# Kernel tuning notes

Measured on AMD Instinct MI355X. Metric: run time of the kernel, lower is better.

## Reference

```python
import jax, jax.numpy as jnp
import numpy as np

L, B, C, H = 1024, 8, 1024, 16
D = C // H  # 64


def setup_inputs() -> dict:
    key = jax.random.key(0)
    ks = jax.random.split(key, 8)
    hidden_states = jax.random.normal(ks[0], (L, B, C), dtype=jnp.float32)
    rotary_pos_emb = jax.random.uniform(ks[1], (L, D // 2), dtype=jnp.float32) * 10.0
    attention_mask = jax.random.randint(ks[2], (B, L, L), 0, 2) > 0
    s = 1.0 / np.sqrt(C)
    Wqkv = jax.random.uniform(ks[3], (3 * C, C), dtype=jnp.float32, minval=-s, maxval=s)
    bqkv = jax.random.uniform(ks[4], (3 * C,), dtype=jnp.float32, minval=-s, maxval=s)
    Wo = jax.random.uniform(ks[5], (C, C), dtype=jnp.float32, minval=-s, maxval=s)
    bo = jax.random.uniform(ks[6], (C,), dtype=jnp.float32, minval=-s, maxval=s)
    return {"hidden_states": hidden_states, "rotary_pos_emb": rotary_pos_emb,
            "attention_mask": attention_mask, "Wqkv": Wqkv, "bqkv": bqkv, "Wo": Wo, "bo": bo}


def _rotate_half(x):
    # interleaved pairs: [-x1, x0, -x3, x2, ...]
    x2 = x.reshape(*x.shape[:-1], -1, 2)
    return jnp.stack((-x2[..., 1], x2[..., 0]), axis=-1).reshape(x.shape)


def reference(hidden_states, rotary_pos_emb, attention_mask, Wqkv, bqkv, Wo, bo):
    Lx, Bx, Cx = hidden_states.shape
    # QKV projection: (L,B,3C) -> (3,B,L,H,D)
    qkv = hidden_states @ Wqkv.T + bqkv
    qkv = qkv.reshape(Lx, Bx, 3, H, D).transpose(2, 1, 0, 3, 4)
    q, k, v = qkv[0], qkv[1], qkv[2]  # (B, L, H, D)
    # RoPE: freqs (L, D/2) -> cos/sin (1, L, 1, D) via duplication
    rpe = rotary_pos_emb[None] if rotary_pos_emb.ndim == 2 else rotary_pos_emb
    cos = jnp.concatenate([jnp.cos(rpe), jnp.cos(rpe)], axis=-1)[:, :, None, :]
    sin = jnp.concatenate([jnp.sin(rpe), jnp.sin(rpe)], axis=-1)[:, :, None, :]
    q = q * cos + _rotate_half(q) * sin
    k = k * cos + _rotate_half(k) * sin
    # (B, H, L, D)
    q = q.transpose(0, 2, 1, 3)
    k = k.transpose(0, 2, 1, 3)
    v = v.transpose(0, 2, 1, 3)
    scale = 1.0 / jnp.sqrt(jnp.asarray(D, dtype=q.dtype))
    scores = jnp.einsum('bhqd,bhkd->bhqk', q, k) * scale
    # torch SDPA bool mask: True = attend, False = masked
    scores = jnp.where(attention_mask[:, None, :, :], scores, jnp.finfo(scores.dtype).min)
    attn = jax.nn.softmax(scores, axis=-1)
    out = jnp.einsum('bhqk,bhkd->bhqd', attn, v)  # (B, H, L, D)
    out = out.transpose(2, 0, 1, 3).reshape(Lx, Bx, Cx)  # (L, B, C)
    return out @ Wo.T + bo
```

## Files before the change

### kernel.cpp

```cpp
#include <hip/hip_runtime.h>
#include <hip/hip_bf16.h>

typedef short bf16x8 __attribute__((ext_vector_type(8)));
typedef short bf16x4 __attribute__((ext_vector_type(4)));
typedef float f32x4 __attribute__((ext_vector_type(4)));
typedef unsigned int u32;
typedef unsigned long long u64;

#define GLD_LDS16(gp, lp) \
  __builtin_amdgcn_global_load_lds((const __attribute__((address_space(1))) u32*)(gp), \
                                   (__attribute__((address_space(3))) u32*)(lp), 16, 0, 0)

__device__ __forceinline__ short f2bf(float f) {
  u32 u = __builtin_bit_cast(u32, f);
  u = (u + 0x7fffu + ((u >> 16) & 1u)) >> 16;
  return (short)u;
}

__device__ __forceinline__ u32 pack2_bf16(float a, float b) {
#if __has_builtin(__builtin_amdgcn_cvt_pk_bf16_f32)
  typedef __bf16 bf16v2 __attribute__((ext_vector_type(2)));
  bf16v2 r = __builtin_amdgcn_cvt_pk_bf16_f32(a, b);
  return __builtin_bit_cast(u32, r);
#else
  u32 r;
  asm("v_cvt_pk_bf16_f32 %0, %1, %2" : "=v"(r) : "v"(a), "v"(b));
  return r;
#endif
}

__device__ __forceinline__ float exp2_fast(float x) {
#if __has_builtin(__builtin_amdgcn_exp2f)
  return __builtin_amdgcn_exp2f(x);
#else
  return exp2f(x);
#endif
}


__global__ __launch_bounds__(256) void cvt_all(
    const float* __restrict__ hs, const float* __restrict__ wqkv,
    const float* __restrict__ wo, short* __restrict__ xb,
    short* __restrict__ wqkvb, short* __restrict__ wob) {
  int b = blockIdx.x;
  const float* in;
  short* out;
  int base;
  if (b < 8192) {
    in = hs; out = xb; base = b * 1024;
  } else if (b < 8192 + 3072) {
    in = wqkv; out = wqkvb; base = (b - 8192) * 1024;
  } else {
    in = wo; out = wob; base = (b - 11264) * 1024;
  }
  int i = base + threadIdx.x * 4;
  float4 v = *(const float4*)(in + i);
  short4 o;
  o.x = f2bf(v.x); o.y = f2bf(v.y); o.z = f2bf(v.z); o.w = f2bf(v.w);
  *(short4*)(out + i) = o;
}

__global__ void rope_tables(const float* __restrict__ rpe, float* __restrict__ cosT,
                            float* __restrict__ sinT) {
  int i = blockIdx.x * 256 + threadIdx.x;
  float v = rpe[i];
  cosT[i] = cosf(v);
  sinT[i] = sinf(v);
}

__global__ void mask_pack(const int* __restrict__ m, u64* __restrict__ out) {
  int i = blockIdx.x * 256 + threadIdx.x;
  u64 bm = __ballot(m[i] != 0);
  if ((threadIdx.x & 63) == 0) out[i >> 6] = bm;
}

__global__ __launch_bounds__(256, 4) void gemm_qkv(
    const short* __restrict__ Xb, const short* __restrict__ Wb,
    const float* __restrict__ bqkv, const float* __restrict__ cosT,
    const float* __restrict__ sinT, short* __restrict__ qb,
    short* __restrict__ kbuf, short* __restrict__ vbuf) {
  __shared__ short Ash[2][128 * 32];
  __shared__ short Bsh[2][128 * 32];
  const int tid = threadIdx.x;
  const int wid = tid >> 6, lane = tid & 63;
  const int g = lane >> 4, c = lane & 15;
  const int wm = wid >> 1, wn = wid & 1;
  const int m0 = blockIdx.y * 128, n0 = blockIdx.x * 128;

  f32x4 acc[4][4];
  for (int i = 0; i < 4; i++)
    for (int j = 0; j < 4; j++) acc[i][j] = (f32x4){0.f, 0.f, 0.f, 0.f};

  const int srow = lane >> 2;
  const int scol = ((lane & 3) ^ ((lane >> 3) & 3)) * 8;
  const short* AgL = Xb + (long)(m0 + wid * 32 + srow) * 1024 + scol;
  const short* BgL = Wb + (long)(n0 + wid * 32 + srow) * 1024 + scol;
  const int dst0 = (wid * 32) * 32;
  const int dst1 = (wid * 32 + 16) * 32;
  const int ck = g ^ ((c >> 1) & 3);

#define QKV_KSTEP(CA, CB, PA, PB, nko) do { \
    GLD_LDS16(AgL + (nko), &(PA)[dst0]); \
    GLD_LDS16(AgL + (nko) + 16 * 1024, &(PA)[dst1]); \
    GLD_LDS16(BgL + (nko), &(PB)[dst0]); \
    GLD_LDS16(BgL + (nko) + 16 * 1024, &(PB)[dst1]); \
    asm volatile("s_waitcnt vmcnt(4)" ::: "memory"); \
    __builtin_amdgcn_s_barrier(); \
    __builtin_amdgcn_sched_barrier(0); \
    bf16x8 af[4], bfr[4]; \
    for (int i = 0; i < 4; i++) \
      af[i] = *(const bf16x8*)&(CA)[(wm * 64 + i * 16 + c) * 32 + ck * 8]; \
    for (int j = 0; j < 4; j++) \
      bfr[j] = *(const bf16x8*)&(CB)[(wn * 64 + j * 16 + c) * 32 + ck * 8]; \
    for (int i = 0; i < 4; i++) \
      for (int j = 0; j < 4; j++) \
        acc[i][j] = __builtin_amdgcn_mfma_f32_16x16x32_bf16(bfr[j], af[i], acc[i][j], 0, 0, 0); \
    __builtin_amdgcn_sched_barrier(0); \
    __builtin_amdgcn_s_barrier(); \
  } while (0)

  GLD_LDS16(AgL, &Ash[0][dst0]);
  GLD_LDS16(AgL + 16 * 1024, &Ash[0][dst1]);
  GLD_LDS16(BgL, &Bsh[0][dst0]);
  GLD_LDS16(BgL + 16 * 1024, &Bsh[0][dst1]);
  for (int kt = 0; kt < 32; kt += 2) {
    QKV_KSTEP(Ash[0], Bsh[0], Ash[1], Bsh[1], (kt + 1) * 32);
    QKV_KSTEP(Ash[1], Bsh[1], Ash[0], Bsh[0], ((kt + 2) & 31) * 32);
  }
#undef QKV_KSTEP

  for (int jt = 0; jt < 4; jt++) {
    const int chan = n0 + wn * 64 + jt * 16 + g * 4;
    const int three = chan >> 10;
    const int hh = (chan >> 6) & 15;
    const int d = chan & 63;
    const float4 bq = *(const float4*)&bqkv[chan];
    for (int i = 0; i < 4; i++) {
      const int r = m0 + wm * 64 + i * 16 + c;
      const int l = r >> 3, b = r & 7;
      float v0 = acc[i][jt][0] + bq.x;
      float v1 = acc[i][jt][1] + bq.y;
      float v2 = acc[i][jt][2] + bq.z;
      float v3 = acc[i][jt][3] + bq.w;
      const long doff = ((long)(b * 16 + hh) * 1024 + l) * 64 + d;
      if (three == 2) {
        uint2 o = {pack2_bf16(v0, v1), pack2_bf16(v2, v3)};
        *(uint2*)&vbuf[doff] = o;
      } else {
        const float4 cs = *(const float4*)&cosT[l * 32 + (d & 31)];
        const float4 sn = *(const float4*)&sinT[l * 32 + (d & 31)];
        float e0 = v0 * cs.x - v1 * sn.x;
        float o0 = v1 * cs.y + v0 * sn.y;
        float e1 = v2 * cs.z - v3 * sn.z;
        float o1 = v3 * cs.w + v2 * sn.w;
        short* dst;
        if (three == 0) {
          const float S = 0.18033688011f;
          e0 *= S; o0 *= S; e1 *= S; o1 *= S;
          dst = qb;
        } else {
          dst = kbuf;
        }
        uint2 o = {pack2_bf16(e0, o0), pack2_bf16(e1, o1)};
        *(uint2*)&dst[doff] = o;
      }
    }
  }
}

__global__ __launch_bounds__(256) void transpose_v(const short* __restrict__ vbuf,
                                                   short* __restrict__ vTb) {
  __shared__ short T[64 * 72];
  const int bh = blockIdx.y;
  const int l0 = blockIdx.x * 64;
  const int t = threadIdx.x;
  const int row = t >> 3;
  const int cc = (t & 7) * 8;
  const short* src = vbuf + ((long)bh * 1024 + l0) * 64;
  for (int p = 0; p < 2; p++) {
    int lr = row + p * 32;
    *(bf16x8*)&T[lr * 72 + cc] = *(const bf16x8*)&src[(long)lr * 64 + cc];
  }
  __syncthreads();
  short* dst = vTb + (long)bh * 64 * 1024 + l0;
  for (int p = 0; p < 2; p++) {
    int d = row + p * 32;
    bf16x8 v;
    for (int j = 0; j < 8; j++) v[j] = T[(cc + j) * 72 + d];
    *(bf16x8*)&dst[(long)d * 1024 + cc] = v;
  }
}

__global__ __launch_bounds__(256, 5) void flash_attn(
    const short* __restrict__ qb, const short* __restrict__ kbuf,
    const short* __restrict__ vTb, const u64* __restrict__ maskb,
    short* __restrict__ attno) {
  __shared__ short K0[64 * 64], K1[64 * 64];
  __shared__ short V0[64 * 64], V1[64 * 64];
  const int t = threadIdx.x;
  const int wid = t >> 6, lane = t & 63;
  const int g = lane >> 4, c = lane & 15;
  const int q0 = blockIdx.x * 64;
  const int bh = blockIdx.y;
  const int b = bh >> 4;
  const int h = bh & 15;
  const long qoff = (long)bh * 1024 * 64;
  const int qrow = q0 + wid * 16 + c;

  bf16x8 aq0, aq1;
  {
    const short* qp = qb + qoff + (long)qrow * 64;
    aq0 = *(const bf16x8*)(qp + g * 8);
    aq1 = *(const bf16x8*)(qp + 32 + g * 8);
  }

  f32x4 Od[4];
  for (int i = 0; i < 4; i++) Od[i] = (f32x4){0.f, 0.f, 0.f, 0.f};
  f32x4 Ld = (f32x4){0.f, 0.f, 0.f, 0.f};
  float m_run = -1e30f;

  bf16x8 avOnes8;
  {
    union { bf16x8 v; u32 u[4]; } av;
    u32 o1 = (c == 0) ? 0x3F803F80u : 0u;
    av.u[0] = av.u[1] = av.u[2] = av.u[3] = o1;
    avOnes8 = av.v;
  }

  const u64* mrow = maskb + ((long)b * 1024 + qrow) * 16;
  const short* Kg = kbuf + qoff;
  const short* Vg = vTb + qoff;

  const int l8 = lane >> 3, l7 = lane & 7;
  const int sr = wid * 16 + l8;
  const int sch = ((l7 ^ l8) & 7) * 8;
  const int r1 = wid * 16 + l8;
  const int r2 = r1 + 8;
  const int kp1 = (r1 & 32) | (((r1 & 15) >> 2) << 3) | (((r1 >> 4) & 1) << 2) | (r1 & 3);
  const int kp2 = (r2 & 32) | (((r2 & 15) >> 2) << 3) | (((r2 >> 4) & 1) << 2) | (r2 & 3);

  const int ck0 = g ^ (c & 7);
  const int kOff0 = c * 64 + ck0 * 8;
  const int kOff1 = c * 64 + (ck0 ^ 4) * 8;
  int vOff32[2];
  for (int kg = 0; kg < 2; kg++)
    vOff32[kg] = c * 64 + (((kg * 4 + g) ^ (c & 7)) * 8);

#define STAGE(KD, VD, ktn) do { \
    GLD_LDS16(Kg + (long)((ktn) + kp1) * 64 + sch,      &KD[(wid * 16) * 64]); \
    GLD_LDS16(Kg + (long)((ktn) + kp2) * 64 + sch,      &KD[(wid * 16 + 8) * 64]); \
    GLD_LDS16(Vg + (long)sr * 1024 + (ktn) + sch,       &VD[(wid * 16) * 64]); \
    GLD_LDS16(Vg + (long)(sr + 8) * 1024 + (ktn) + sch, &VD[(wid * 16 + 8) * 64]); \
  } while (0)

#define TILE(KB, VB, KP, VP, ki) do { \
    u64 mw = mrow[ki];  \
    __syncthreads();  \
    STAGE(KP, VP, (((ki) + 1) & 15) * 64); \
    f32x4 z[4]; \
    for (int nt = 0; nt < 4; nt++) { \
      bf16x8 bk0 = *(const bf16x8*)&KB[kOff0 + nt * 1024]; \
      bf16x8 bk1 = *(const bf16x8*)&KB[kOff1 + nt * 1024]; \
      f32x4 zz = (f32x4){0.f, 0.f, 0.f, 0.f}; \
      zz = __builtin_amdgcn_mfma_f32_16x16x32_bf16(bk0, aq0, zz, 0, 0, 0); \
      zz = __builtin_amdgcn_mfma_f32_16x16x32_bf16(bk1, aq1, zz, 0, 0, 0); \
      z[nt] = zz; \
    } \
    float mx = fmaxf(fmaxf(fmaxf(z[0][0], z[0][1]), fmaxf(z[0][2], z[0][3])), \
                     fmaxf(fmaxf(z[1][0], z[1][1]), fmaxf(z[1][2], z[1][3]))); \
    mx = fmaxf(mx, fmaxf(fmaxf(fmaxf(z[2][0], z[2][1]), fmaxf(z[2][2], z[2][3])), \
                         fmaxf(fmaxf(z[3][0], z[3][1]), fmaxf(z[3][2], z[3][3])))); \
    if (__ballot(mx > m_run + 8.f)) {  \
      mx = fmaxf(mx, __shfl_xor(mx, 16, 64)); \
      mx = fmaxf(mx, __shfl_xor(mx, 32, 64)); \
      float mnew = fmaxf(m_run, mx); \
      float al = exp2_fast(m_run - mnew); \
      for (int dt = 0; dt < 4; dt++) { \
        Od[dt][0] *= al; Od[dt][1] *= al; Od[dt][2] *= al; Od[dt][3] *= al; \
      } \
      Ld[0] *= al; \
      m_run = mnew; \
    } \
    for (int kg = 0; kg < 2; kg++) { \
      union { bf16x8 v; u32 u[4]; } pu; \
      for (int ntp = 0; ntp < 2; ntp++) { \
        const int nt = kg * 2 + ntp; \
        u32 m4 = (u32)(mw >> (kg * 32 + g * 8 + ntp * 4)) & 0xFu; \
        u32 mlo = ((m4 & 1u) ? 0xFFFFu : 0u) | ((m4 & 2u) ? 0xFFFF0000u : 0u); \
        u32 mhi = ((m4 & 4u) ? 0xFFFFu : 0u) | ((m4 & 8u) ? 0xFFFF0000u : 0u); \
        float p0 = exp2_fast(z[nt][0] - m_run); \
        float p1 = exp2_fast(z[nt][1] - m_run); \
        float p2 = exp2_fast(z[nt][2] - m_run); \
        float p3 = exp2_fast(z[nt][3] - m_run); \
        pu.u[ntp * 2 + 0] = pack2_bf16(p0, p1) & mlo; \
        pu.u[ntp * 2 + 1] = pack2_bf16(p2, p3) & mhi; \
      } \
      Ld = __builtin_amdgcn_mfma_f32_16x16x32_bf16(avOnes8, pu.v, Ld, 0, 0, 0); \
      for (int dt = 0; dt < 4; dt++) { \
        bf16x8 av = *(const bf16x8*)&VB[vOff32[kg] + dt * 1024]; \
        Od[dt] = __builtin_amdgcn_mfma_f32_16x16x32_bf16(av, pu.v, Od[dt], 0, 0, 0); \
      } \
    } \
  } while (0)

  STAGE(K0, V0, 0);
  for (int ki = 0; ki < 16; ki += 2) {
    TILE(K0, V0, K1, V1, ki);
    TILE(K1, V1, K0, V0, ki + 1);
  }
#undef TILE
#undef STAGE

  float lsum = __shfl(Ld[0], c, 64);
  float inv = 1.f / lsum;
  long rbase = ((long)qrow * 8 + b) * 1024 + h * 64 + g * 4;
  for (int dt = 0; dt < 4; dt++) {
    union { bf16x4 v; u32 u[2]; } o;
    o.u[0] = pack2_bf16(Od[dt][0] * inv, Od[dt][1] * inv);
    o.u[1] = pack2_bf16(Od[dt][2] * inv, Od[dt][3] * inv);
    *(bf16x4*)&attno[rbase + dt * 16] = o.v;
  }
}

__global__ __launch_bounds__(256, 4) void gemm_out(
    const short* __restrict__ Ab, const short* __restrict__ Wob,
    const float* __restrict__ bo, float* __restrict__ out) {
  __shared__ short Ash[2][128 * 32];
  __shared__ short Bsh[2][128 * 32];
  const int tid = threadIdx.x;
  const int wid = tid >> 6, lane = tid & 63;
  const int g = lane >> 4, c = lane & 15;
  const int wm = wid >> 1, wn = wid & 1;
  const int m0 = blockIdx.y * 128, n0 = blockIdx.x * 128;

  f32x4 acc[4][4];
  for (int i = 0; i < 4; i++)
    for (int j = 0; j < 4; j++) acc[i][j] = (f32x4){0.f, 0.f, 0.f, 0.f};

  const int srow = lane >> 2;
  const int scol = ((lane & 3) ^ ((lane >> 3) & 3)) * 8;
  const short* AgL = Ab + (long)(m0 + wid * 32 + srow) * 1024 + scol;
  const short* BgL = Wob + (long)(n0 + wid * 32 + srow) * 1024 + scol;
  const int dst0 = (wid * 32) * 32;
  const int dst1 = (wid * 32 + 16) * 32;
  const int ck = g ^ ((c >> 1) & 3);

#define OUT_KSTEP(CA, CB, PA, PB, nko) do { \
    GLD_LDS16(AgL + (nko), &(PA)[dst0]); \
    GLD_LDS16(AgL + (nko) + 16 * 1024, &(PA)[dst1]); \
    GLD_LDS16(BgL + (nko), &(PB)[dst0]); \
    GLD_LDS16(BgL + (nko) + 16 * 1024, &(PB)[dst1]); \
    asm volatile("s_waitcnt vmcnt(4)" ::: "memory"); \
    __builtin_amdgcn_s_barrier(); \
    __builtin_amdgcn_sched_barrier(0); \
    bf16x8 af[4], bfr[4]; \
    for (int i = 0; i < 4; i++) \
      af[i] = *(const bf16x8*)&(CA)[(wm * 64 + i * 16 + c) * 32 + ck * 8]; \
    for (int j = 0; j < 4; j++) \
      bfr[j] = *(const bf16x8*)&(CB)[(wn * 64 + j * 16 + c) * 32 + ck * 8]; \
    for (int i = 0; i < 4; i++) \
      for (int j = 0; j < 4; j++) \
        acc[i][j] = __builtin_amdgcn_mfma_f32_16x16x32_bf16(af[i], bfr[j], acc[i][j], 0, 0, 0); \
    __builtin_amdgcn_sched_barrier(0); \
    __builtin_amdgcn_s_barrier(); \
  } while (0)

  GLD_LDS16(AgL, &Ash[0][dst0]);
  GLD_LDS16(AgL + 16 * 1024, &Ash[0][dst1]);
  GLD_LDS16(BgL, &Bsh[0][dst0]);
  GLD_LDS16(BgL + 16 * 1024, &Bsh[0][dst1]);
  for (int kt = 0; kt < 32; kt += 2) {
    OUT_KSTEP(Ash[0], Bsh[0], Ash[1], Bsh[1], (kt + 1) * 32);
    OUT_KSTEP(Ash[1], Bsh[1], Ash[0], Bsh[0], ((kt + 2) & 31) * 32);
  }
#undef OUT_KSTEP

  for (int jt = 0; jt < 4; jt++) {
    const int j = n0 + wn * 64 + jt * 16 + c;
    const float bias = bo[j];
    for (int i = 0; i < 4; i++) {
      const int rbase = m0 + wm * 64 + i * 16 + g * 4;
      for (int reg = 0; reg < 4; reg++)
        out[(long)(rbase + reg) * 1024 + j] = acc[i][jt][reg] + bias;
    }
  }
}

extern "C" void kernel_launch(void* const* d_in, const int* in_sizes, int n_in,
                              void* d_out, int out_size, void* d_ws, size_t ws_size,
                              hipStream_t stream) {
  const float* hs = (const float*)d_in[0];
  const float* rpe = (const float*)d_in[1];
  const int* amask = (const int*)d_in[2];
  const float* Wqkv = (const float*)d_in[3];
  const float* bqkv = (const float*)d_in[4];
  const float* Wo = (const float*)d_in[5];
  const float* bo = (const float*)d_in[6];
  float* out = (float*)d_out;

  char* ws = (char*)d_ws;
  auto alloc = [&](size_t bytes) {
    char* p = ws;
    ws += (bytes + 255) & ~(size_t)255;
    return p;
  };
  short* Xb = (short*)alloc(8192LL * 1024 * 2);
  short* Wqkvb = (short*)alloc(3072LL * 1024 * 2);
  short* Wob = (short*)alloc(1024LL * 1024 * 2);
  float* cosT = (float*)alloc(1024 * 32 * 4);
  float* sinT = (float*)alloc(1024 * 32 * 4);
  u64* maskb = (u64*)alloc(8LL * 1024 * 16 * 8);
  short* qb = (short*)alloc(128LL * 1024 * 64 * 2);
  short* kbuf = (short*)alloc(128LL * 1024 * 64 * 2);
  short* vbuf = (short*)alloc(128LL * 1024 * 64 * 2);
  short* vTb = (short*)alloc(128LL * 1024 * 64 * 2);
  short* attno = (short*)alloc(8192LL * 1024 * 2);

  cvt_all<<<12288, 256, 0, stream>>>(hs, Wqkv, Wo, Xb, Wqkvb, Wob);
  rope_tables<<<128, 256, 0, stream>>>(rpe, cosT, sinT);
  mask_pack<<<32768, 256, 0, stream>>>(amask, maskb);
  gemm_qkv<<<dim3(24, 64), 256, 0, stream>>>(Xb, Wqkvb, bqkv, cosT, sinT, qb, kbuf, vbuf);
  transpose_v<<<dim3(16, 128), 256, 0, stream>>>(vbuf, vTb);
  flash_attn<<<dim3(16, 128), 256, 0, stream>>>(qb, kbuf, vTb, maskb, attno);
  gemm_out<<<dim3(8, 64), 256, 0, stream>>>(attno, Wob, bo, out);
}
```

Baseline: 326.4 us.

## Fuse prep kernels, swizzle block order, and restructure GEMM LDS pipelining

Merges the three preprocessing kernels (mask packing, bf16 conversion, RoPE tables) into one launch to cut launch overhead. Remaps block indices in both GEMMs and the attention kernel with an XCD-style swizzle (bid&7 stride) so that blocks sharing operands land on the same die's L2. Replaces the hand-tuned vmcnt wait plus raw barrier double buffer in the GEMMs with a stage/compute split separated by __syncthreads. That split may serialize load completion more conservatively, because __syncthreads drains all outstanding loads.

```diff
diff --git a/kernel.cpp b/kernel.cpp
--- a/kernel.cpp
+++ b/kernel.cpp
@@ -37,41 +37,44 @@
 #endif
 }
 
-
-__global__ __launch_bounds__(256) void cvt_all(
+__global__ __launch_bounds__(256) void prep_all(
+    const int* __restrict__ m, u64* __restrict__ maskb,
     const float* __restrict__ hs, const float* __restrict__ wqkv,
     const float* __restrict__ wo, short* __restrict__ xb,
-    short* __restrict__ wqkvb, short* __restrict__ wob) {
+    short* __restrict__ wqkvb, short* __restrict__ wob,
+    const float* __restrict__ rpe, float* __restrict__ cosT,
+    float* __restrict__ sinT) {
   int b = blockIdx.x;
-  const float* in;
-  short* out;
-  int base;
-  if (b < 8192) {
-    in = hs; out = xb; base = b * 1024;
-  } else if (b < 8192 + 3072) {
-    in = wqkv; out = wqkvb; base = (b - 8192) * 1024;
-  } else {
-    in = wo; out = wob; base = (b - 11264) * 1024;
-  }
-  int i = base + threadIdx.x * 4;
-  float4 v = *(const float4*)(in + i);
-  short4 o;
-  o.x = f2bf(v.x); o.y = f2bf(v.y); o.z = f2bf(v.z); o.w = f2bf(v.w);
-  *(short4*)(out + i) = o;
-}
-
-__global__ void rope_tables(const float* __restrict__ rpe, float* __restrict__ cosT,
-                            float* __restrict__ sinT) {
-  int i = blockIdx.x * 256 + threadIdx.x;
+  if (b < 32768) {
+    int i = b * 256 + threadIdx.x;
+    u64 bm = __ballot(m[i] != 0);
+    if ((threadIdx.x & 63) == 0) maskb[i >> 6] = bm;
+    return;
+  }
+  b -= 32768;
+  if (b < 12288) {
+    const float* in;
+    short* out;
+    int base;
+    if (b < 8192) {
+      in = hs; out = xb; base = b * 1024;
+    } else if (b < 8192 + 3072) {
+      in = wqkv; out = wqkvb; base = (b - 8192) * 1024;
+    } else {
+      in = wo; out = wob; base = (b - 11264) * 1024;
+    }
+    int i = base + threadIdx.x * 4;
+    float4 v = *(const float4*)(in + i);
+    short4 o;
+    o.x = f2bf(v.x); o.y = f2bf(v.y); o.z = f2bf(v.z); o.w = f2bf(v.w);
+    *(short4*)(out + i) = o;
+    return;
+  }
+  b -= 12288;
+  int i = b * 256 + threadIdx.x;
   float v = rpe[i];
   cosT[i] = cosf(v);
   sinT[i] = sinf(v);
-}
-
-__global__ void mask_pack(const int* __restrict__ m, u64* __restrict__ out) {
-  int i = blockIdx.x * 256 + threadIdx.x;
-  u64 bm = __ballot(m[i] != 0);
-  if ((threadIdx.x & 63) == 0) out[i >> 6] = bm;
 }
 
 __global__ __launch_bounds__(256, 4) void gemm_qkv(
@@ -85,7 +88,9 @@
   const int wid = tid >> 6, lane = tid & 63;
   const int g = lane >> 4, c = lane & 15;
   const int wm = wid >> 1, wn = wid & 1;
-  const int m0 = blockIdx.y * 128, n0 = blockIdx.x * 128;
+  const int bid = blockIdx.y * 24 + blockIdx.x;
+  const int swz = (bid & 7) * 192 + (bid >> 3);
+  const int m0 = (swz / 24) * 128, n0 = (swz % 24) * 128;
 
   f32x4 acc[4][4];
   for (int i = 0; i < 4; i++)
@@ -99,14 +104,14 @@
   const int dst1 = (wid * 32 + 16) * 32;
   const int ck = g ^ ((c >> 1) & 3);
 
-#define QKV_KSTEP(CA, CB, PA, PB, nko) do { \
+#define QKV_STAGE(PA, PB, nko) do { \
     GLD_LDS16(AgL + (nko), &(PA)[dst0]); \
     GLD_LDS16(AgL + (nko) + 16 * 1024, &(PA)[dst1]); \
     GLD_LDS16(BgL + (nko), &(PB)[dst0]); \
     GLD_LDS16(BgL + (nko) + 16 * 1024, &(PB)[dst1]); \
-    asm volatile("s_waitcnt vmcnt(4)" ::: "memory"); \
-    __builtin_amdgcn_s_barrier(); \
-    __builtin_amdgcn_sched_barrier(0); \
+  } while (0)
+
+#define QKV_COMPUTE(CA, CB) do { \
     bf16x8 af[4], bfr[4]; \
     for (int i = 0; i < 4; i++) \
       af[i] = *(const bf16x8*)&(CA)[(wm * 64 + i * 16 + c) * 32 + ck * 8]; \
@@ -115,19 +120,20 @@
     for (int i = 0; i < 4; i++) \
       for (int j = 0; j < 4; j++) \
         acc[i][j] = __builtin_amdgcn_mfma_f32_16x16x32_bf16(bfr[j], af[i], acc[i][j], 0, 0, 0); \
-    __builtin_amdgcn_sched_barrier(0); \
-    __builtin_amdgcn_s_barrier(); \
-  } while (0)
-
-  GLD_LDS16(AgL, &Ash[0][dst0]);
-  GLD_LDS16(AgL + 16 * 1024, &Ash[0][dst1]);
-  GLD_LDS16(BgL, &Bsh[0][dst0]);
-  GLD_LDS16(BgL + 16 * 1024, &Bsh[0][dst1]);
+  } while (0)
+
+  QKV_STAGE(Ash[0], Bsh[0], 0);
+  __syncthreads();
   for (int kt = 0; kt < 32; kt += 2) {
-    QKV_KSTEP(Ash[0], Bsh[0], Ash[1], Bsh[1], (kt + 1) * 32);
-    QKV_KSTEP(Ash[1], Bsh[1], Ash[0], Bsh[0], ((kt + 2) & 31) * 32);
-  }
-#undef QKV_KSTEP
+    QKV_STAGE(Ash[1], Bsh[1], (kt + 1) * 32);
+    QKV_COMPUTE(Ash[0], Bsh[0]);
+    __syncthreads();
+    if (kt + 2 < 32) QKV_STAGE(Ash[0], Bsh[0], (kt + 2) * 32);
+    QKV_COMPUTE(Ash[1], Bsh[1]);
+    __syncthreads();
+  }
+#undef QKV_STAGE
+#undef QKV_COMPUTE
 
   for (int jt = 0; jt < 4; jt++) {
     const int chan = n0 + wn * 64 + jt * 16 + g * 4;
@@ -200,8 +206,10 @@
   const int t = threadIdx.x;
   const int wid = t >> 6, lane = t & 63;
   const int g = lane >> 4, c = lane & 15;
-  const int q0 = blockIdx.x * 64;
-  const int bh = blockIdx.y;
+  const int bid = blockIdx.y * 16 + blockIdx.x;
+  const int swz = (bid & 7) * 256 + (bid >> 3);
+  const int q0 = (swz & 15) * 64;
+  const int bh = swz >> 4;
   const int b = bh >> 4;
   const int h = bh & 15;
   const long qoff = (long)bh * 1024 * 64;
@@ -331,7 +339,9 @@
   const int wid = tid >> 6, lane = tid & 63;
   const int g = lane >> 4, c = lane & 15;
   const int wm = wid >> 1, wn = wid & 1;
-  const int m0 = blockIdx.y * 128, n0 = blockIdx.x * 128;
+  const int bid = blockIdx.y * 8 + blockIdx.x;
+  const int swz = (bid & 7) * 64 + (bid >> 3);
+  const int m0 = (swz >> 3) * 128, n0 = (swz & 7) * 128;
 
   f32x4 acc[4][4];
   for (int i = 0; i < 4; i++)
@@ -345,14 +355,14 @@
   const int dst1 = (wid * 32 + 16) * 32;
   const int ck = g ^ ((c >> 1) & 3);
 
-#define OUT_KSTEP(CA, CB, PA, PB, nko) do { \
+#define OUT_STAGE(PA, PB, nko) do { \
     GLD_LDS16(AgL + (nko), &(PA)[dst0]); \
     GLD_LDS16(AgL + (nko) + 16 * 1024, &(PA)[dst1]); \
     GLD_LDS16(BgL + (nko), &(PB)[dst0]); \
     GLD_LDS16(BgL + (nko) + 16 * 1024, &(PB)[dst1]); \
-    asm volatile("s_waitcnt vmcnt(4)" ::: "memory"); \
-    __builtin_amdgcn_s_barrier(); \
-    __builtin_amdgcn_sched_barrier(0); \
+  } while (0)
+
+#define OUT_COMPUTE(CA, CB) do { \
     bf16x8 af[4], bfr[4]; \
     for (int i = 0; i < 4; i++) \
       af[i] = *(const bf16x8*)&(CA)[(wm * 64 + i * 16 + c) * 32 + ck * 8]; \
@@ -361,19 +371,20 @@
     for (int i = 0; i < 4; i++) \
       for (int j = 0; j < 4; j++) \
         acc[i][j] = __builtin_amdgcn_mfma_f32_16x16x32_bf16(af[i], bfr[j], acc[i][j], 0, 0, 0); \
-    __builtin_amdgcn_sched_barrier(0); \
-    __builtin_amdgcn_s_barrier(); \
-  } while (0)
-
-  GLD_LDS16(AgL, &Ash[0][dst0]);
-  GLD_LDS16(AgL + 16 * 1024, &Ash[0][dst1]);
-  GLD_LDS16(BgL, &Bsh[0][dst0]);
-  GLD_LDS16(BgL + 16 * 1024, &Bsh[0][dst1]);
+  } while (0)
+
+  OUT_STAGE(Ash[0], Bsh[0], 0);
+  __syncthreads();
   for (int kt = 0; kt < 32; kt += 2) {
-    OUT_KSTEP(Ash[0], Bsh[0], Ash[1], Bsh[1], (kt + 1) * 32);
-    OUT_KSTEP(Ash[1], Bsh[1], Ash[0], Bsh[0], ((kt + 2) & 31) * 32);
-  }
-#undef OUT_KSTEP
+    OUT_STAGE(Ash[1], Bsh[1], (kt + 1) * 32);
+    OUT_COMPUTE(Ash[0], Bsh[0]);
+    __syncthreads();
+    if (kt + 2 < 32) OUT_STAGE(Ash[0], Bsh[0], (kt + 2) * 32);
+    OUT_COMPUTE(Ash[1], Bsh[1]);
+    __syncthreads();
+  }
+#undef OUT_STAGE
+#undef OUT_COMPUTE
 
   for (int jt = 0; jt < 4; jt++) {
     const int j = n0 + wn * 64 + jt * 16 + c;
@@ -416,9 +427,8 @@
   short* vTb = (short*)alloc(128LL * 1024 * 64 * 2);
   short* attno = (short*)alloc(8192LL * 1024 * 2);
 
-  cvt_all<<<12288, 256, 0, stream>>>(hs, Wqkv, Wo, Xb, Wqkvb, Wob);
-  rope_tables<<<128, 256, 0, stream>>>(rpe, cosT, sinT);
-  mask_pack<<<32768, 256, 0, stream>>>(amask, maskb);
+  prep_all<<<45184, 256, 0, stream>>>(amask, maskb, hs, Wqkv, Wo, Xb, Wqkvb, Wob,
+                                      rpe, cosT, sinT);
   gemm_qkv<<<dim3(24, 64), 256, 0, stream>>>(Xb, Wqkvb, bqkv, cosT, sinT, qb, kbuf, vbuf);
   transpose_v<<<dim3(16, 128), 256, 0, stream>>>(vbuf, vTb);
   flash_attn<<<dim3(16, 128), 256, 0, stream>>>(qb, kbuf, vTb, maskb, attno);
```

After: 314.3 us. -3.7%, faster.
